# Kernel optimization log

Measured on AMD Instinct MI355X. Metric: run time of the kernel, lower is better.

## Reference

```python
import jax, jax.numpy as jnp
import numpy as np

GROUP = 32  # quantization group size along K, fixed by the call site


def setup_inputs() -> dict:
    key = jax.random.key(0)
    k1, k2, k3 = jax.random.split(key, 3)
    M, K, N = 1, 8192, 16384
    A = jax.random.normal(k1, (M, K), dtype=jnp.float16)
    # packed int4 weights: each byte holds two nibbles -> [N, K//2]
    B = jax.random.randint(k2, (N, K // 2), 0, 256, dtype=jnp.int32)
    scalesAndZeros = (jax.random.normal(k3, (N, K // GROUP, 2), dtype=jnp.float16))
    return {"A": A, "B": B, "scalesAndZeros": scalesAndZeros}


def _dequant(B, scalesAndZeros):
    # B: [N, K//2] bytes, two int4 values per byte (low nibble = even k)
    N, Kh = B.shape
    K = Kh * 2
    low = B & 0xF
    high = (B >> 4) & 0xF
    q = jnp.stack([low, high], axis=-1).reshape(N, K).astype(jnp.float32) - 8.0
    scales = scalesAndZeros[..., 0].astype(jnp.float32)  # [N, K//GROUP]
    zeros = scalesAndZeros[..., 1].astype(jnp.float32)   # [N, K//GROUP]
    qg = q.reshape(N, K // GROUP, GROUP)
    W = qg * scales[:, :, None] + zeros[:, :, None]       # [N, K//GROUP, GROUP]
    return W.reshape(N, K)


def reference(A, B, scalesAndZeros):
    # int4 weight-only quantized GEMV: out[m, n] = sum_k A[m, k] * dequant(W)[n, k]
    W = _dequant(B, scalesAndZeros)                        # [N, K] fp32
    out = jnp.einsum("mk,nk->mn", A.astype(jnp.float32), W)
    return out.astype(A.dtype)                             # [1, N] fp16
```

## Files before the change

kernel.cpp:

```cpp
#include <hip/hip_runtime.h>
#include <hip/hip_bf16.h>


__global__ __launch_bounds__(256) void gemv_w4(
    const float4* __restrict__ A4,
    const int4*   __restrict__ B,
    const float2* __restrict__ SZ,
    float* __restrict__ out,
    int groups_per_row,
    int N)
{
    const int n = blockIdx.x;
    if (n >= N) return;
    const int t = threadIdx.x;

    const float2 sz = SZ[(size_t)n * groups_per_row + t];
    const float s = sz.x;
    const float z = sz.y;

    const int4*   Bp = B  + (size_t)n * (groups_per_row * 4) + t * 4;
    const float4* Ap = A4 + t * 8;

    float dot = 0.0f;
    float sA  = 0.0f;
#pragma unroll
    for (int j = 0; j < 4; ++j) {
        const int4   b  = Bp[j];
        const float4 a0 = Ap[2 * j];
        const float4 a1 = Ap[2 * j + 1];
        const int   bb[4] = { b.x, b.y, b.z, b.w };
        const float aa[8] = { a0.x, a0.y, a0.z, a0.w, a1.x, a1.y, a1.z, a1.w };
#pragma unroll
        for (int m = 0; m < 4; ++m) {
            const float alo = aa[2 * m];
            const float ahi = aa[2 * m + 1];
            dot = fmaf(alo, (float)(bb[m] & 0xF), dot);
            dot = fmaf(ahi, (float)((bb[m] >> 4) & 0xF), dot);
            sA += alo + ahi;
        }
    }
    float part = fmaf(s, dot, (z - 8.0f * s) * sA);

#pragma unroll
    for (int off = 32; off > 0; off >>= 1)
        part += __shfl_down(part, off, 64);

    __shared__ float red[4];
    if ((t & 63) == 0) red[t >> 6] = part;
    __syncthreads();
    if (t == 0) {
        out[n] = red[0] + red[1] + red[2] + red[3];
    }
}

extern "C" void kernel_launch(void* const* d_in, const int* in_sizes, int n_in,
                              void* d_out, int out_size, void* d_ws, size_t ws_size,
                              hipStream_t stream) {
    const float4* A4 = (const float4*)d_in[0];
    const int4*   B  = (const int4*)d_in[1];
    const float2* SZ = (const float2*)d_in[2];
    float* out = (float*)d_out;

    const int N = out_size;
    const int Kh = in_sizes[1] / N;
    const int groups = (2 * Kh) / 32;

    gemv_w4<<<N, 256, 0, stream>>>(A4, B, SZ, out, groups, N);
}
```

Measured before the change: 428.0 us.

## Process eight rows per block, keep A in registers, coalesce B loads

Each block now handles eight output rows instead of one. The activation slice and its per-group sums are loaded into registers once and reused across all eight rows. The B indexing changes so that consecutive threads read consecutive int4 words, and the scale reads are reindexed to match. The row sums are reduced together with a single barrier. The cost is hardcoded row strides (1024 int4s for B, 256 groups per row) and no guard on the row index in the loop, which ties the kernel to K=8192 and N divisible by 8, along with more register pressure and fewer blocks.

```diff
diff --git a/kernel.cpp b/kernel.cpp
--- a/kernel.cpp
+++ b/kernel.cpp
@@ -2,54 +2,74 @@
 #include <hip/hip_bf16.h>
 
 
-__global__ __launch_bounds__(256) void gemv_w4(
+#define ROWS 8
+
+__global__ __launch_bounds__(256) void gemv_w4r(
     const float4* __restrict__ A4,
     const int4*   __restrict__ B,
     const float2* __restrict__ SZ,
     float* __restrict__ out,
-    int groups_per_row,
     int N)
 {
-    const int n = blockIdx.x;
-    if (n >= N) return;
-    const int t = threadIdx.x;
+    const int t  = threadIdx.x;
+    const int n0 = blockIdx.x * ROWS;
 
-    const float2 sz = SZ[(size_t)n * groups_per_row + t];
-    const float s = sz.x;
-    const float z = sz.y;
-
-    const int4*   Bp = B  + (size_t)n * (groups_per_row * 4) + t * 4;
-    const float4* Ap = A4 + t * 8;
-
-    float dot = 0.0f;
-    float sA  = 0.0f;
+    float a[4][8];
+    float sAj[4];
 #pragma unroll
     for (int j = 0; j < 4; ++j) {
-        const int4   b  = Bp[j];
-        const float4 a0 = Ap[2 * j];
-        const float4 a1 = Ap[2 * j + 1];
-        const int   bb[4] = { b.x, b.y, b.z, b.w };
-        const float aa[8] = { a0.x, a0.y, a0.z, a0.w, a1.x, a1.y, a1.z, a1.w };
+        const float4 x = A4[2 * t + 512 * j];
+        const float4 y = A4[2 * t + 512 * j + 1];
+        a[j][0] = x.x; a[j][1] = x.y; a[j][2] = x.z; a[j][3] = x.w;
+        a[j][4] = y.x; a[j][5] = y.y; a[j][6] = y.z; a[j][7] = y.w;
+        sAj[j] = ((x.x + x.y) + (x.z + x.w)) + ((y.x + y.y) + (y.z + y.w));
+    }
+
+    __shared__ float red[ROWS][4];
+    const int lane = t & 63;
+    const int w    = t >> 6;
+
+    float acc[ROWS];
 #pragma unroll
-        for (int m = 0; m < 4; ++m) {
-            const float alo = aa[2 * m];
-            const float ahi = aa[2 * m + 1];
-            dot = fmaf(alo, (float)(bb[m] & 0xF), dot);
-            dot = fmaf(ahi, (float)((bb[m] >> 4) & 0xF), dot);
-            sA += alo + ahi;
+    for (int r = 0; r < ROWS; ++r) acc[r] = 0.0f;
+
+    for (int r = 0; r < ROWS; ++r) {
+        const int n = n0 + r;
+        const int4*   Bp = B  + (size_t)n * 1024;
+        const float2* Sp = SZ + (size_t)n * 256 + (t >> 2);
+
+        float part = 0.0f;
+#pragma unroll
+        for (int j = 0; j < 4; ++j) {
+            const int4   b  = Bp[t + 256 * j];
+            const float2 sz = Sp[64 * j];
+            const int bb[4] = { b.x, b.y, b.z, b.w };
+            float dot = 0.0f;
+#pragma unroll
+            for (int m = 0; m < 4; ++m) {
+                dot = fmaf(a[j][2 * m],     (float)(bb[m] & 0xF),        dot);
+                dot = fmaf(a[j][2 * m + 1], (float)((bb[m] >> 4) & 0xF), dot);
+            }
+            const float zz = fmaf(-8.0f, sz.x, sz.y);
+            part = fmaf(sz.x, dot, part);
+            part = fmaf(zz, sAj[j], part);
         }
+        acc[r] = part;
     }
-    float part = fmaf(s, dot, (z - 8.0f * s) * sA);
 
 #pragma unroll
-    for (int off = 32; off > 0; off >>= 1)
-        part += __shfl_down(part, off, 64);
-
-    __shared__ float red[4];
-    if ((t & 63) == 0) red[t >> 6] = part;
+    for (int r = 0; r < ROWS; ++r) {
+        float v = acc[r];
+#pragma unroll
+        for (int off = 32; off > 0; off >>= 1)
+            v += __shfl_down(v, off, 64);
+        if (lane == 0) red[r][w] = v;
+    }
     __syncthreads();
-    if (t == 0) {
-        out[n] = red[0] + red[1] + red[2] + red[3];
+    if (t < ROWS) {
+        const int n = n0 + t;
+        if (n < N)
+            out[n] = (red[t][0] + red[t][1]) + (red[t][2] + red[t][3]);
     }
 }
 
@@ -62,8 +82,5 @@
     float* out = (float*)d_out;
 
     const int N = out_size;
-    const int Kh = in_sizes[1] / N;
-    const int groups = (2 * Kh) / 32;
-
-    gemv_w4<<<N, 256, 0, stream>>>(A4, B, SZ, out, groups, N);
+    gemv_w4r<<<N / ROWS, 256, 0, stream>>>(A4, B, SZ, out, N);
 }
```

Measured after the change: 373.5 us. 1.15x faster.
